# Optimization experiments

Measured on AMD Instinct MI355X. Metric: run time of the kernel, lower is better.

The kernel has to match this reference:

```python
import jax, jax.numpy as jnp
import numpy as np

WEIGHT = 0.1
TEMPERATURE = 0.07
EPS_NORM = 1e-12   # F.normalize eps
EPS_DEN = 1e-6     # denominator eps in pos_mask.sum()


def setup_inputs() -> dict:
    key = jax.random.key(0)
    k1, k2 = jax.random.split(key)
    features = jax.random.normal(k1, (4, 1000, 2048), dtype=jnp.float32)
    target = jax.random.randint(k2, (4, 1000), 0, 16, dtype=jnp.int64)
    return {"features": features, "target": target}


def _per_sample_loss(f, t):
    # f: [N, C], t: [N]
    N = f.shape[0]
    # F.normalize(dim=1)
    norm = jnp.maximum(jnp.linalg.norm(f, axis=1, keepdims=True), EPS_NORM)
    f = f / norm
    # [N, N] cosine similarities scaled by temperature
    sim = jnp.matmul(f, f.T) / TEMPERATURE
    eye = jnp.eye(N, dtype=f.dtype)
    pos = (t[:, None] == t[None, :]).astype(f.dtype) * (1.0 - eye)
    neg = 1.0 - pos - eye
    pos_sim = sim * pos
    # -log(exp(pos_sim) / (exp(pos_sim) + sum_j exp(sim)*neg))  summed over ALL entries
    denom = jnp.exp(pos_sim) + jnp.sum(jnp.exp(sim) * neg, axis=1, keepdims=True)
    loss_mat = jnp.log(denom) - pos_sim
    pos_sum = pos.sum()
    return loss_mat.sum() / (pos_sum + EPS_DEN), pos_sum


def reference(features, target):
    # features: [B, N, C] (already 3-D: no subsampling / interpolation paths fire)
    losses, pos_sums = jax.vmap(_per_sample_loss)(features, target)
    valid = pos_sums > 0
    num_pairs = valid.sum().astype(features.dtype)
    total = jnp.where(valid, losses, 0.0).sum()
    return jnp.where(num_pairs > 0, WEIGHT * total / num_pairs,
                     jnp.asarray(WEIGHT * 0.1, dtype=features.dtype))
```

## Files before the change

### kernel.cpp

```cpp
#include <hip/hip_runtime.h>
#include <hip/hip_fp8.h>
#include <math.h>

#define BB 4
#define NN 1000
#define NP 1024
#define CC 2048
#define TINV (1.0f / 0.07f)
#define BK 64
#define FS 8.0f
#define PVCAP 160

#define FNORM_BYTES ((size_t)BB * NP * CC)
#define SIMB_BYTES  ((size_t)2 * BB * NP * NP)
#define RL_BYTES    ((size_t)BB * NP * 4)

typedef unsigned char u8;
typedef float  f32x4  __attribute__((ext_vector_type(4)));
typedef float  f32x16 __attribute__((ext_vector_type(16)));
typedef int    i32x8  __attribute__((ext_vector_type(8)));

#define SC1 0x7F7F7F7F

__device__ __forceinline__ void load_lds16(const void* g, void* l) {
    __builtin_amdgcn_global_load_lds(
        (const __attribute__((address_space(1))) unsigned int*)g,
        (__attribute__((address_space(3))) unsigned int*)l, 16, 0, 0);
}

__device__ __forceinline__ float blk_sum(float v, volatile float* lds) {
    int lane = threadIdx.x & 63;
    int wid  = threadIdx.x >> 6;
#pragma unroll
    for (int off = 32; off; off >>= 1) v += __shfl_down(v, off);
    __syncthreads();
    if (lane == 0) lds[wid] = v;
    __syncthreads();
    return lds[0] + lds[1] + lds[2] + lds[3];
}

__device__ __forceinline__ float wave_sum(float v) {
#pragma unroll
    for (int off = 32; off; off >>= 1) v += __shfl_down(v, off);
    return __shfl(v, 0);
}

__device__ __forceinline__ float fp8_to_f32(u8 b) {
    __hip_fp8_e4m3 q; q.__x = b;
    return (float)q;
}

__device__ __forceinline__ i32x8 frag32(const u8* row, int c0, int c1) {
    int4 lo = *(const int4*)(row + c0 * 16);
    int4 hi = *(const int4*)(row + c1 * 16);
    i32x8 r = {lo.x, lo.y, lo.z, lo.w, hi.x, hi.y, hi.z, hi.w};
    return r;
}

__global__ __launch_bounds__(256) void norm_fp8_kernel(const float* __restrict__ f,
                                                       u8* __restrict__ out) {
    __shared__ float lds[4];
    __shared__ float scale_s;
    const int blk = blockIdx.x;
    const int b = blk >> 10, r = blk & (NP - 1);
    u8* dst = out + ((size_t)b * NP + r) * CC;
    const int tid = threadIdx.x;

    if (r >= NN) {
        ((uint2*)dst)[tid] = make_uint2(0u, 0u);
        return;
    }
    const float* src = f + ((size_t)b * NN + r) * CC;

    float4 v0 = ((const float4*)src)[tid * 2];
    float4 v1 = ((const float4*)src)[tid * 2 + 1];
    float ss = v0.x * v0.x + v0.y * v0.y + v0.z * v0.z + v0.w * v0.w
             + v1.x * v1.x + v1.y * v1.y + v1.z * v1.z + v1.w * v1.w;
    float tot = blk_sum(ss, lds);
    if (tid == 0) scale_s = FS / fmaxf(sqrtf(tot), 1e-12f);
    __syncthreads();
    const float sc = scale_s;

    float x[8] = {v0.x, v0.y, v0.z, v0.w, v1.x, v1.y, v1.z, v1.w};
    union { u8 b[8]; uint2 u; } pk;
#pragma unroll
    for (int k = 0; k < 8; ++k) {
        __hip_fp8_e4m3 q(x[k] * sc);
        pk.b[k] = q.__x;
    }
    ((uint2*)dst)[tid] = pk.u;
}

__global__ __launch_bounds__(256) void simgemm_mfma(const u8* __restrict__ fn,
                                                    u8* __restrict__ simb) {
    __shared__ __align__(16) u8 As0[128 * BK], As1[128 * BK];
    __shared__ __align__(16) u8 Bs0[128 * BK], Bs1[128 * BK];

    const int bz = blockIdx.z;
    const int b  = bz >> 1;
    const int kbeg = (bz & 1) * (CC / 2);
    const int tI = blockIdx.y * 128;
    const int tJ = blockIdx.x * 128;
    const u8* base = fn + (size_t)b * NP * CC;
    u8* S = simb + (size_t)bz * NP * NP;

    const int tid  = threadIdx.x;
    const int wid  = tid >> 6;
    const int lane = tid & 63;
    const int wm   = wid >> 1;
    const int wn   = wid & 1;
    const int ln32 = lane & 31;
    const int kh   = lane >> 5;
    const int sw   = (ln32 >> 1) & 3;
    const int c0   = (kh * 2)     ^ sw;
    const int c1   = (kh * 2 + 1) ^ sw;

    const int srow   = tid >> 2;
    const int schunk = (tid & 3) ^ ((srow >> 1) & 3);
    const u8* gA = base + (size_t)(tI + srow) * CC + kbeg + schunk * 16;
    const u8* gB = base + (size_t)(tJ + srow) * CC + kbeg + schunk * 16;
    const int wvoff = wid * 1024;

    f32x16 acc[2][2] = {};

#define STAGE(k0, A, B)                                            \
    {                                                              \
        load_lds16(gA + (k0),                   (A) + wvoff);      \
        load_lds16(gA + (k0) + (size_t)64 * CC, (A) + 4096 + wvoff); \
        load_lds16(gB + (k0),                   (B) + wvoff);      \
        load_lds16(gB + (k0) + (size_t)64 * CC, (B) + 4096 + wvoff); \
    }

#define COMPUTE(A, B)                                                         \
    {                                                                         \
        const u8* Ar0 = (A) + (wm * 64      + ln32) * BK;                     \
        const u8* Ar1 = (A) + (wm * 64 + 32 + ln32) * BK;                     \
        const u8* Br0 = (B) + (wn * 64      + ln32) * BK;                     \
        const u8* Br1 = (B) + (wn * 64 + 32 + ln32) * BK;                     \
        i32x8 a0 = frag32(Ar0, c0, c1);                                       \
        i32x8 a1 = frag32(Ar1, c0, c1);                                       \
        i32x8 b0 = frag32(Br0, c0, c1);                                       \
        i32x8 b1 = frag32(Br1, c0, c1);                                       \
        acc[0][0] = __builtin_amdgcn_mfma_scale_f32_32x32x64_f8f6f4(          \
            a0, b0, acc[0][0], 0, 0, 0, SC1, 0, SC1);                         \
        acc[0][1] = __builtin_amdgcn_mfma_scale_f32_32x32x64_f8f6f4(          \
            a0, b1, acc[0][1], 0, 0, 0, SC1, 0, SC1);                         \
        acc[1][0] = __builtin_amdgcn_mfma_scale_f32_32x32x64_f8f6f4(          \
            a1, b0, acc[1][0], 0, 0, 0, SC1, 0, SC1);                         \
        acc[1][1] = __builtin_amdgcn_mfma_scale_f32_32x32x64_f8f6f4(          \
            a1, b1, acc[1][1], 0, 0, 0, SC1, 0, SC1);                         \
    }

    STAGE(0, As0, Bs0);
#pragma unroll 1
    for (int k0 = 0; k0 < CC / 2; k0 += 2 * BK) {
        __syncthreads();
        if (k0 + BK < CC / 2) STAGE(k0 + BK, As1, Bs1);
        COMPUTE(As0, Bs0);
        __syncthreads();
        if (k0 + 2 * BK < CC / 2) STAGE(k0 + 2 * BK, As0, Bs0);
        COMPUTE(As1, Bs1);
    }
#undef STAGE
#undef COMPUTE

    const float oscale = TINV / (FS * FS);
#pragma unroll
    for (int at = 0; at < 2; ++at) {
#pragma unroll
        for (int bt = 0; bt < 2; ++bt) {
            const int col = tJ + wn * 64 + bt * 32 + ln32;
#pragma unroll
            for (int r = 0; r < 16; ++r) {
                const int row = tI + wm * 64 + at * 32 + (r & 3) + 8 * (r >> 2) + 4 * kh;
                __hip_fp8_e4m3 q(acc[at][bt][r] * oscale);
                S[(size_t)row * NP + col] = q.__x;
            }
        }
    }
}

__global__ __launch_bounds__(256) void rowloss_kernel(const u8* __restrict__ simb,
                                                      const int* __restrict__ tgt,
                                                      float* __restrict__ rloss,
                                                      float* __restrict__ rpos) {
    __shared__ __align__(16) int ts[NN];
    __shared__ float pv[4][PVCAP];
    const int b = blockIdx.y;
    const int wid = threadIdx.x >> 6, lane = threadIdx.x & 63;
    const int* t = tgt + (size_t)b * NN;
    for (int j = threadIdx.x; j < NN; j += 256) ts[j] = t[j];
    __syncthreads();

    const int i = blockIdx.x * 4 + wid;
    const u8* r0 = simb + (size_t)(2 * b) * NP * NP + (size_t)i * NP;
    const u8* r1 = r0 + (size_t)NP * NP;
    const int ti = ts[i];

    float sneg = 0.f;
    int pbase = 0;
#pragma unroll
    for (int it = 0; it < 2; ++it) {
        const int g = lane + it * 64;
        const bool act = g < NN / 8;
        union { uint2 u; u8 b[8]; } pa, pb;
        pa.u = act ? ((const uint2*)r0)[g] : make_uint2(0u, 0u);
        pb.u = act ? ((const uint2*)r1)[g] : make_uint2(0u, 0u);
        float v[8];
        bool pos[8];
        const int jb = g * 8;
#pragma unroll
        for (int k = 0; k < 8; ++k) {
            v[k] = fp8_to_f32(pa.b[k]) + fp8_to_f32(pb.b[k]);
            const int j = jb + k;
            const bool ok = act && (j != i);
            pos[k] = ok && (ts[act ? j : 0] == ti);
            if (ok && !pos[k]) sneg += __expf(v[k]);
        }
#pragma unroll
        for (int k = 0; k < 8; ++k) {
            const unsigned long long m = __ballot(pos[k]);
            if (pos[k]) {
                const int rank = __popcll(m & ((1ull << lane) - 1ull));
                const int slot = pbase + rank;
                if (slot < PVCAP) pv[wid][slot] = v[k];
            }
            pbase += (int)__popcll(m);
        }
    }
    const float S = wave_sum(sneg);

    float term = 0.f;
    for (int k = lane; k < pbase; k += 64) {
        const float s = pv[wid][k];
        term += __logf(__expf(s) + S) - s;
    }
    const float tt = wave_sum(term);
    if (lane == 0) {
        rloss[b * NP + i] = tt + ((float)NN - (float)pbase) * __logf(1.f + S);
        rpos [b * NP + i] = (float)pbase;
    }
}

__global__ __launch_bounds__(256) void final_kernel(const float* __restrict__ rloss,
                                                    const float* __restrict__ rpos,
                                                    float* __restrict__ out) {
    __shared__ float lds[4];
    float total = 0.f, np = 0.f;
    for (int b = 0; b < BB; ++b) {
        float l = 0.f, p = 0.f;
        for (int i = threadIdx.x; i < NN; i += 256) {
            l += rloss[b * NP + i];
            p += rpos [b * NP + i];
        }
        float ls = blk_sum(l, lds);
        float ps = blk_sum(p, lds);
        if (ps > 0.f) { total += ls / (ps + 1e-6f); np += 1.f; }
    }
    if (threadIdx.x == 0)
        out[0] = (np > 0.f) ? 0.1f * total / np : 0.1f * 0.1f;
}

extern "C" void kernel_launch(void* const* d_in, const int* in_sizes, int n_in,
                              void* d_out, int out_size, void* d_ws, size_t ws_size,
                              hipStream_t stream) {
    const float* feat = (const float*)d_in[0];
    const int*   tgt  = (const int*)d_in[1];
    char* ws = (char*)d_ws;
    u8*    fnorm = (u8*)ws;                       ws += FNORM_BYTES;
    u8*    simb  = (u8*)ws;                       ws += SIMB_BYTES;
    float* rloss = (float*)ws;                    ws += RL_BYTES;
    float* rpos  = (float*)ws;

    norm_fp8_kernel<<<dim3(BB * NP), 256, 0, stream>>>(feat, fnorm);
    simgemm_mfma<<<dim3(NP / 128, NP / 128, 2 * BB), 256, 0, stream>>>(fnorm, simb);
    rowloss_kernel<<<dim3(NN / 4, BB), 256, 0, stream>>>(simb, tgt, rloss, rpos);
    final_kernel<<<1, 256, 0, stream>>>(rloss, rpos, (float*)d_out);
}
```

Measured before the change: 106.3 us.

## Exploit Gram matrix symmetry: compute upper-triangular tiles and mirror-store transposes

The similarity GEMM now launches only the 36 upper-triangular 128x128 tiles per batch and split-K half instead of all 64, mapping a linear block index to (ti,tj). Off-diagonal tiles additionally write their transposed result, packing 4 consecutive fp8 rows into 32-bit stores. This is meant to cut the MFMA work and feature loads by nearly half. In exchange it adds extra scattered transpose stores and a small index-decoding loop.

```diff
diff --git a/kernel.cpp b/kernel.cpp
--- a/kernel.cpp
+++ b/kernel.cpp
@@ -96,13 +96,18 @@
     __shared__ __align__(16) u8 As0[128 * BK], As1[128 * BK];
     __shared__ __align__(16) u8 Bs0[128 * BK], Bs1[128 * BK];
 
-    const int bz = blockIdx.z;
-    const int b  = bz >> 1;
-    const int kbeg = (bz & 1) * (CC / 2);
-    const int tI = blockIdx.y * 128;
-    const int tJ = blockIdx.x * 128;
+    int u = blockIdx.x;
+    int ti = 0;
+    while (u >= 8 - ti) { u -= 8 - ti; ++ti; }
+    const int tj = ti + u;
+    const int tI = ti * 128;
+    const int tJ = tj * 128;
+
+    const int kz = blockIdx.y;
+    const int b  = blockIdx.z;
+    const int kbeg = kz * (CC / 2);
     const u8* base = fn + (size_t)b * NP * CC;
-    u8* S = simb + (size_t)bz * NP * NP;
+    u8* S = simb + (size_t)(b * 2 + kz) * NP * NP;
 
     const int tid  = threadIdx.x;
     const int wid  = tid >> 6;
@@ -165,16 +170,29 @@
 #undef COMPUTE
 
     const float oscale = TINV / (FS * FS);
+    const bool offdiag = (tI != tJ);
 #pragma unroll
     for (int at = 0; at < 2; ++at) {
 #pragma unroll
         for (int bt = 0; bt < 2; ++bt) {
             const int col = tJ + wn * 64 + bt * 32 + ln32;
+            union { u8 b[16]; unsigned int w[4]; } qq;
+#pragma unroll
+            for (int r = 0; r < 16; ++r) {
+                __hip_fp8_e4m3 q(acc[at][bt][r] * oscale);
+                qq.b[r] = q.__x;
+            }
 #pragma unroll
             for (int r = 0; r < 16; ++r) {
                 const int row = tI + wm * 64 + at * 32 + (r & 3) + 8 * (r >> 2) + 4 * kh;
-                __hip_fp8_e4m3 q(acc[at][bt][r] * oscale);
-                S[(size_t)row * NP + col] = q.__x;
+                S[(size_t)row * NP + col] = qq.b[r];
+            }
+            if (offdiag) {
+#pragma unroll
+                for (int q4 = 0; q4 < 4; ++q4) {
+                    const int rowb = tI + wm * 64 + at * 32 + 8 * q4 + 4 * kh;
+                    *(unsigned int*)&S[(size_t)col * NP + rowb] = qq.w[q4];
+                }
             }
         }
     }
@@ -273,7 +291,7 @@
     float* rpos  = (float*)ws;
 
     norm_fp8_kernel<<<dim3(BB * NP), 256, 0, stream>>>(feat, fnorm);
-    simgemm_mfma<<<dim3(NP / 128, NP / 128, 2 * BB), 256, 0, stream>>>(fnorm, simb);
+    simgemm_mfma<<<dim3(36, 2, BB), 256, 0, stream>>>(fnorm, simb);
     rowloss_kernel<<<dim3(NN / 4, BB), 256, 0, stream>>>(simb, tgt, rloss, rpos);
     final_kernel<<<1, 256, 0, stream>>>(rloss, rpos, (float*)d_out);
 }
```

Result: no change. 107.2 us (+0.9%).
